# Kernel optimization log

Hardware: AMD Instinct MI355X
Metric: run time of the kernel (lower is better)

The kernel has to match this reference:

```python
import jax, jax.numpy as jnp
from jax import lax
import numpy as np

# kz = (7, 3): kh is a 1x7 horizontal kernel, kv is a 3x1 vertical kernel
KH = (1, 7)
KV = (3, 1)


def _morph(x, ksz, op, init):
    # F.unfold zero-pads, so padded border values participate in the min/max
    ph, pw = ksz[0] // 2, ksz[1] // 2
    xp = jnp.pad(x, ((0, 0), (0, 0), (ph, ph), (pw, pw)))
    return lax.reduce_window(xp, init, op, (1, 1, ksz[0], ksz[1]), (1, 1, 1, 1), 'VALID')


def _erode(x, ksz):
    return _morph(x, ksz, lax.min, np.float32(np.inf))


def _dilate(x, ksz):
    return _morph(x, ksz, lax.max, np.float32(-np.inf))


def _calphi(x):
    dil = _dilate(x, KH)                                   # horizontal dilation (1x7)
    thr = dil.mean(axis=(2, 3), keepdims=True)             # per-image mean of dilation
    bi = ((x > thr) & (x == dil)).astype(x.dtype)          # horizontal local-max binarization
    return _dilate(_erode(bi, KV), KV)                     # morphological opening with 3x1


def setup_inputs() -> dict:
    key = jax.random.key(0)
    x = jax.random.normal(key, (8, 1, 2048, 2048), dtype=jnp.float32)
    return {"x": x}


def reference(x):
    s1 = _calphi(x).sum()
    s2 = _calphi(jnp.swapaxes(x, 2, 3)).sum()
    return s1 < s2
```

## Files before the change

kernel.cpp:

```cpp
#include <hip/hip_runtime.h>
#include <cstdint>

#define NEG_INF (-__builtin_inff())

static constexpr int H = 2048;
static constexpr int W = 2048;
static constexpr int STR = 248;
static constexpr int RC  = 16;
static constexpr int NR  = RC + 6;
static constexpr int NCH = H / RC;
static constexpr int GY  = NCH / 4;
static constexpr int NBLK = 9 * GY * 8;

struct F4 { float x, y, z, w; };

__device__ __forceinline__ F4 ld4(const float* __restrict__ p) {
    float4 v = *reinterpret_cast<const float4*>(p);
    return {v.x, v.y, v.z, v.w};
}

__device__ __forceinline__ float fmax3(float a, float b, float c) {
    return fmaxf(fmaxf(a, b), c);
}

__device__ __forceinline__ void hmax7_4(float a0, float a1, float a2,
                                        float a3, float a4, float a5, float a6,
                                        float a7, float a8, float a9,
                                        float& m0, float& m1, float& m2, float& m3) {
    float p23 = fmaxf(a2, a3), p45 = fmaxf(a4, a5), p67 = fmaxf(a6, a7);
    float q25 = fmaxf(p23, p45), q47 = fmaxf(p45, p67);
    m0 = fmax3(fmaxf(a0, a1), q25, a6);
    m1 = fmax3(fmaxf(a1, a2), fmax3(a3, a4, a5), fmaxf(a6, a7));
    m2 = fmax3(p23, q47, a8);
    m3 = fmax3(fmaxf(a3, a4), fmax3(a5, a6, a7), fmaxf(a8, a9));
}

struct Setup {
    int c4, cA, cmask, imask;
    float pad0, pad1, pad2, pad3;
};

__device__ __forceinline__ Setup make_setup(int sIdx, int lane) {
    Setup s;
    const int cstart = sIdx * STR;
    s.c4 = cstart - 4 + lane * 4;
    s.cA = min(max(s.c4, 0), W - 4);
    s.cmask = 0; s.imask = 0;
#pragma unroll
    for (int k = 0; k < 4; ++k) {
        const int col = s.c4 + k;
        if (col >= cstart && col < cstart + STR && col < W) s.cmask |= 1 << k;
        if (col >= 0 && col < W)                            s.imask |= 1 << k;
    }
    s.pad0 = ((s.c4 + 0) < 3 || (s.c4 + 0) > W - 4) ? 0.f : NEG_INF;
    s.pad1 = ((s.c4 + 1) < 3 || (s.c4 + 1) > W - 4) ? 0.f : NEG_INF;
    s.pad2 = ((s.c4 + 2) < 3 || (s.c4 + 2) > W - 4) ? 0.f : NEG_INF;
    s.pad3 = ((s.c4 + 3) < 3 || (s.c4 + 3) > W - 4) ? 0.f : NEG_INF;
    return s;
}

__device__ __forceinline__ void load_rows(const float* __restrict__ img,
                                          int r0, const Setup& s, F4 (&cur)[NR]) {
#pragma unroll
    for (int t = 0; t < NR; ++t) {
        const int irc = min(max(r0 - 3 + t, 0), H - 1);
        cur[t] = ld4(img + (size_t)irc * W + s.cA);
    }
#pragma unroll
    for (int t = 0; t < NR; ++t)
        asm volatile("" : "+v"(cur[t].x), "+v"(cur[t].y), "+v"(cur[t].z), "+v"(cur[t].w));
    if (s.imask != 0xF) {
#pragma unroll
        for (int t = 0; t < NR; ++t) {
            if (!(s.imask & 1)) cur[t].x = NEG_INF;
            if (!(s.imask & 2)) cur[t].y = NEG_INF;
            if (!(s.imask & 4)) cur[t].z = NEG_INF;
            if (!(s.imask & 8)) cur[t].w = NEG_INF;
        }
    }
#pragma unroll
    for (int t = 0; t < NR; ++t) {
        if (t < 3 || t >= NR - 3) {
            const int ir = r0 - 3 + t;
            if (ir < 0 || ir >= H) cur[t] = {NEG_INF, NEG_INF, NEG_INF, NEG_INF};
        }
    }
}

__device__ __forceinline__ int blk_id() {
    return (blockIdx.z * GY + blockIdx.y) * 9 + blockIdx.x;
}

__global__ __launch_bounds__(256) void k_sums(const float* __restrict__ x,
                                              double* __restrict__ sums) {
    const int tid = threadIdx.x, lane = tid & 63, wid = tid >> 6;
    const int sIdx = blockIdx.x;
    const int rr   = blockIdx.y * 4 + wid;
    const int b    = blockIdx.z;
    const int r0   = rr * RC;
    const float* img = x + (size_t)b * H * W;
    const Setup s = make_setup(sIdx, lane);

    F4 cur[NR];
    load_rows(img, r0, s, cur);

    float shf = 0.f, svf = 0.f;
#pragma unroll
    for (int t = 3; t < 3 + RC; ++t) {
        F4 c = cur[t];
        float la1 = __shfl_up(c.y, 1), la2 = __shfl_up(c.z, 1), la3 = __shfl_up(c.w, 1);
        float ra0 = __shfl_down(c.x, 1), ra1 = __shfl_down(c.y, 1), ra2 = __shfl_down(c.z, 1);
        float m0, m1, m2, m3;
        hmax7_4(la1, la2, la3, c.x, c.y, c.z, c.w, ra0, ra1, ra2, m0, m1, m2, m3);
        m0 = fmaxf(m0, s.pad0); m1 = fmaxf(m1, s.pad1);
        m2 = fmaxf(m2, s.pad2); m3 = fmaxf(m3, s.pad3);
        shf += ((s.cmask & 1) ? m0 : 0.f) + ((s.cmask & 2) ? m1 : 0.f)
             + ((s.cmask & 4) ? m2 : 0.f) + ((s.cmask & 8) ? m3 : 0.f);
    }
#pragma unroll
    for (int jj = 0; jj < RC; ++jj) {
        const int j = r0 + jj;
        const float rpad = (j < 3 || j > H - 4) ? 0.f : NEG_INF;
        float mx = fmax3(fmax3(cur[jj].x, cur[jj+1].x, cur[jj+2].x),
                         fmax3(cur[jj+3].x, cur[jj+4].x, cur[jj+5].x), cur[jj+6].x);
        float my = fmax3(fmax3(cur[jj].y, cur[jj+1].y, cur[jj+2].y),
                         fmax3(cur[jj+3].y, cur[jj+4].y, cur[jj+5].y), cur[jj+6].y);
        float mz = fmax3(fmax3(cur[jj].z, cur[jj+1].z, cur[jj+2].z),
                         fmax3(cur[jj+3].z, cur[jj+4].z, cur[jj+5].z), cur[jj+6].z);
        float mw = fmax3(fmax3(cur[jj].w, cur[jj+1].w, cur[jj+2].w),
                         fmax3(cur[jj+3].w, cur[jj+4].w, cur[jj+5].w), cur[jj+6].w);
        mx = fmaxf(mx, rpad); my = fmaxf(my, rpad);
        mz = fmaxf(mz, rpad); mw = fmaxf(mw, rpad);
        svf += ((s.cmask & 1) ? mx : 0.f) + ((s.cmask & 2) ? my : 0.f)
             + ((s.cmask & 4) ? mz : 0.f) + ((s.cmask & 8) ? mw : 0.f);
    }

    double sh = (double)shf, sv = (double)svf;
    for (int off = 32; off > 0; off >>= 1) {
        sh += __shfl_down(sh, off);
        sv += __shfl_down(sv, off);
    }
    __shared__ double sdh[4], sdv[4];
    if (lane == 0) { sdh[wid] = sh; sdv[wid] = sv; }
    __syncthreads();
    if (tid == 0) {
        const int blk = blk_id();
        sums[blk]        = sdh[0] + sdh[1] + sdh[2] + sdh[3];
        sums[NBLK + blk] = sdv[0] + sdv[1] + sdv[2] + sdv[3];
    }
}

__global__ void k_thr(const double* __restrict__ sums, float* __restrict__ thr) {
    const int tid = threadIdx.x;
    const int pair = tid >> 4, l16 = tid & 15;
    const double* base = sums + (pair < 8 ? pair * 288 : NBLK + (pair - 8) * 288);
    double a = 0.0;
#pragma unroll
    for (int k = 0; k < 18; ++k) a += base[l16 + k * 16];
    a += __shfl_down(a, 8);
    a += __shfl_down(a, 4);
    a += __shfl_down(a, 2);
    a += __shfl_down(a, 1);
    if (l16 == 0) thr[pair] = (float)(a * (1.0 / ((double)H * (double)W)));
}

__global__ __launch_bounds__(256) void k_counts(const float* __restrict__ x,
                                                const float* __restrict__ thr,
                                                unsigned int* __restrict__ cnts) {
    const int tid = threadIdx.x, lane = tid & 63, wid = tid >> 6;
    const int sIdx = blockIdx.x;
    const int rr   = blockIdx.y * 4 + wid;
    const int b    = blockIdx.z;
    const int r0   = rr * RC;
    const float* img = x + (size_t)b * H * W;
    const Setup s = make_setup(sIdx, lane);
    const float thr1 = thr[b], thr2 = thr[8 + b];

    F4 cur[NR];
    load_rows(img, r0, s, cur);

    unsigned bc0 = 0, bc1 = 0, bc2 = 0, bc3 = 0;
#pragma unroll
    for (int t = 1; t < NR - 1; ++t) {
        F4 c = cur[t];
        float la1 = __shfl_up(c.y, 1), la2 = __shfl_up(c.z, 1), la3 = __shfl_up(c.w, 1);
        float ra0 = __shfl_down(c.x, 1), ra1 = __shfl_down(c.y, 1), ra2 = __shfl_down(c.z, 1);
        float m0, m1, m2, m3;
        hmax7_4(la1, la2, la3, c.x, c.y, c.z, c.w, ra0, ra1, ra2, m0, m1, m2, m3);
        m0 = fmaxf(m0, s.pad0); m1 = fmaxf(m1, s.pad1);
        m2 = fmaxf(m2, s.pad2); m3 = fmaxf(m3, s.pad3);
        bc0 |= (c.x > thr1 && c.x == m0) ? (1u << t) : 0u;
        bc1 |= (c.y > thr1 && c.y == m1) ? (1u << t) : 0u;
        bc2 |= (c.z > thr1 && c.z == m2) ? (1u << t) : 0u;
        bc3 |= (c.w > thr1 && c.w == m3) ? (1u << t) : 0u;
    }
    const unsigned rowm = ((1u << RC) - 1u) << 3;
    unsigned e0 = bc0 & (bc0 << 1) & (bc0 >> 1);
    unsigned e1 = bc1 & (bc1 << 1) & (bc1 >> 1);
    unsigned e2 = bc2 & (bc2 << 1) & (bc2 >> 1);
    unsigned e3 = bc3 & (bc3 << 1) & (bc3 >> 1);
    unsigned o0 = e0 | (e0 << 1) | (e0 >> 1);
    unsigned o1_ = e1 | (e1 << 1) | (e1 >> 1);
    unsigned o2_ = e2 | (e2 << 1) | (e2 >> 1);
    unsigned o3_ = e3 | (e3 << 1) | (e3 >> 1);
    unsigned cnt1 = ((s.cmask & 1) ? __popc(o0  & rowm) : 0u)
                  + ((s.cmask & 2) ? __popc(o1_ & rowm) : 0u)
                  + ((s.cmask & 4) ? __popc(o2_ & rowm) : 0u)
                  + ((s.cmask & 8) ? __popc(o3_ & rowm) : 0u);

    unsigned d0 = 0, d1 = 0, d2 = 0, d3 = 0;
#pragma unroll
    for (int jj = 0; jj < RC; ++jj) {
        const int j = r0 + jj;
        const float rpad = (j < 3 || j > H - 4) ? 0.f : NEG_INF;
        float mx = fmax3(fmax3(cur[jj].x, cur[jj+1].x, cur[jj+2].x),
                         fmax3(cur[jj+3].x, cur[jj+4].x, cur[jj+5].x), cur[jj+6].x);
        float my = fmax3(fmax3(cur[jj].y, cur[jj+1].y, cur[jj+2].y),
                         fmax3(cur[jj+3].y, cur[jj+4].y, cur[jj+5].y), cur[jj+6].y);
        float mz = fmax3(fmax3(cur[jj].z, cur[jj+1].z, cur[jj+2].z),
                         fmax3(cur[jj+3].z, cur[jj+4].z, cur[jj+5].z), cur[jj+6].z);
        float mw = fmax3(fmax3(cur[jj].w, cur[jj+1].w, cur[jj+2].w),
                         fmax3(cur[jj+3].w, cur[jj+4].w, cur[jj+5].w), cur[jj+6].w);
        mx = fmaxf(mx, rpad); my = fmaxf(my, rpad);
        mz = fmaxf(mz, rpad); mw = fmaxf(mw, rpad);
        F4 ce = cur[jj + 3];
        d0 |= (ce.x > thr2 && ce.x == mx) ? (1u << jj) : 0u;
        d1 |= (ce.y > thr2 && ce.y == my) ? (1u << jj) : 0u;
        d2 |= (ce.z > thr2 && ce.z == mz) ? (1u << jj) : 0u;
        d3 |= (ce.w > thr2 && ce.w == mw) ? (1u << jj) : 0u;
    }
    const unsigned pz = __shfl_up(d2, 1), pw = __shfl_up(d3, 1);
    const unsigned n0 = __shfl_down(d0, 1), n1 = __shfl_down(d1, 1);
    const unsigned em1 = pz & pw & d0;
    const unsigned f0  = pw & d0 & d1;
    const unsigned f1  = d0 & d1 & d2;
    const unsigned f2  = d1 & d2 & d3;
    const unsigned f3  = d2 & d3 & n0;
    const unsigned fp4 = d3 & n0 & n1;
    const unsigned q0 = em1 | f0 | f1;
    const unsigned q1 = f0 | f1 | f2;
    const unsigned q2 = f1 | f2 | f3;
    const unsigned q3 = f2 | f3 | fp4;
    unsigned cnt2 = ((s.cmask & 1) ? __popc(q0) : 0u)
                  + ((s.cmask & 2) ? __popc(q1) : 0u)
                  + ((s.cmask & 4) ? __popc(q2) : 0u)
                  + ((s.cmask & 8) ? __popc(q3) : 0u);

    for (int off = 32; off > 0; off >>= 1) {
        cnt1 += __shfl_down(cnt1, off);
        cnt2 += __shfl_down(cnt2, off);
    }
    __shared__ unsigned sc1[4], sc2[4];
    if (lane == 0) { sc1[wid] = cnt1; sc2[wid] = cnt2; }
    __syncthreads();
    if (tid == 0) {
        const int blk = blk_id();
        cnts[blk]        = sc1[0] + sc1[1] + sc1[2] + sc1[3];
        cnts[NBLK + blk] = sc2[0] + sc2[1] + sc2[2] + sc2[3];
    }
}

__global__ void k_final(const unsigned int* __restrict__ cnts,
                        int* __restrict__ out) {
    const int tid = threadIdx.x;
    unsigned a = 0, c = 0;
    for (int i = tid; i < NBLK; i += 256) {
        a += cnts[i];
        c += cnts[NBLK + i];
    }
    for (int off = 32; off > 0; off >>= 1) {
        a += __shfl_down(a, off);
        c += __shfl_down(c, off);
    }
    __shared__ unsigned sa[4], sc[4];
    const int lane = tid & 63, wid = tid >> 6;
    if (lane == 0) { sa[wid] = a; sc[wid] = c; }
    __syncthreads();
    if (tid == 0) {
        unsigned A = sa[0] + sa[1] + sa[2] + sa[3];
        unsigned C = sc[0] + sc[1] + sc[2] + sc[3];
        out[0] = (A < C) ? 1 : 0;
    }
}

extern "C" void kernel_launch(void* const* d_in, const int* in_sizes, int n_in,
                              void* d_out, int out_size, void* d_ws, size_t ws_size,
                              hipStream_t stream) {
    const float* x = (const float*)d_in[0];
    int* out = (int*)d_out;
    double* sums = (double*)d_ws;
    float* thr = (float*)((char*)d_ws + 2 * NBLK * 8);
    unsigned int* cnts = (unsigned int*)((char*)d_ws + 2 * NBLK * 8 + 256);

    k_sums  <<<dim3(9, GY, 8), 256, 0, stream>>>(x, sums);
    k_thr   <<<1, 256, 0, stream>>>(sums, thr);
    k_counts<<<dim3(9, GY, 8), 256, 0, stream>>>(x, thr, cnts);
    k_final <<<1, 256, 0, stream>>>(cnts, out);
}
```

Before: 265.3 us.

## Fold threshold and final reductions into main kernels via atomics; halve row chunk

Removes the two single-block kernels (threshold reduction and final count comparison). Per-block partial sums now go through bucketed double and uint atomics, and every k_counts block recomputes the per-image thresholds from 64 buckets. A last-block-done counter in k_counts produces the final comparison, and a memset clears the workspace. The row chunk drops from 16 to 8, doubling the grid and register-friendly work per wave but increasing halo overhead (14 rows loaded per 8 output rows instead of 22 per 16).

New measurement: 621.1 us. 2.34x slower.

```diff
diff --git a/kernel.cpp b/kernel.cpp
--- a/kernel.cpp
+++ b/kernel.cpp
@@ -6,11 +6,10 @@
 static constexpr int H = 2048;
 static constexpr int W = 2048;
 static constexpr int STR = 248;
-static constexpr int RC  = 16;
+static constexpr int RC  = 8;
 static constexpr int NR  = RC + 6;
-static constexpr int NCH = H / RC;
-static constexpr int GY  = NCH / 4;
-static constexpr int NBLK = 9 * GY * 8;
+static constexpr int GY  = (H / RC) / 4;
+static constexpr int NBLOCKS = 9 * GY * 8;
 
 struct F4 { float x, y, z, w; };
 
@@ -85,10 +84,6 @@
             if (ir < 0 || ir >= H) cur[t] = {NEG_INF, NEG_INF, NEG_INF, NEG_INF};
         }
     }
-}
-
-__device__ __forceinline__ int blk_id() {
-    return (blockIdx.z * GY + blockIdx.y) * 9 + blockIdx.x;
 }
 
 __global__ __launch_bounds__(256) void k_sums(const float* __restrict__ x,
@@ -144,37 +139,39 @@
     if (lane == 0) { sdh[wid] = sh; sdv[wid] = sv; }
     __syncthreads();
     if (tid == 0) {
-        const int blk = blk_id();
-        sums[blk]        = sdh[0] + sdh[1] + sdh[2] + sdh[3];
-        sums[NBLK + blk] = sdv[0] + sdv[1] + sdv[2] + sdv[3];
-    }
-}
-
-__global__ void k_thr(const double* __restrict__ sums, float* __restrict__ thr) {
-    const int tid = threadIdx.x;
-    const int pair = tid >> 4, l16 = tid & 15;
-    const double* base = sums + (pair < 8 ? pair * 288 : NBLK + (pair - 8) * 288);
-    double a = 0.0;
-#pragma unroll
-    for (int k = 0; k < 18; ++k) a += base[l16 + k * 16];
-    a += __shfl_down(a, 8);
-    a += __shfl_down(a, 4);
-    a += __shfl_down(a, 2);
-    a += __shfl_down(a, 1);
-    if (l16 == 0) thr[pair] = (float)(a * (1.0 / ((double)H * (double)W)));
+        const int bkt = (blockIdx.y * 9 + sIdx) & 63;
+        atomicAdd(&sums[(b)     * 64 + bkt], sdh[0] + sdh[1] + sdh[2] + sdh[3]);
+        atomicAdd(&sums[(8 + b) * 64 + bkt], sdv[0] + sdv[1] + sdv[2] + sdv[3]);
+    }
 }
 
 __global__ __launch_bounds__(256) void k_counts(const float* __restrict__ x,
-                                                const float* __restrict__ thr,
-                                                unsigned int* __restrict__ cnts) {
+                                                const double* __restrict__ sums,
+                                                unsigned int* __restrict__ cnts,
+                                                unsigned int* __restrict__ done,
+                                                int* __restrict__ out) {
     const int tid = threadIdx.x, lane = tid & 63, wid = tid >> 6;
+    __shared__ float thrS[16];
+
+    {
+        const int pair = tid >> 4, l16 = tid & 15;
+        const double* bp = sums + pair * 64 + l16;
+        double a = bp[0] + bp[16] + bp[32] + bp[48];
+        a += __shfl_down(a, 8);
+        a += __shfl_down(a, 4);
+        a += __shfl_down(a, 2);
+        a += __shfl_down(a, 1);
+        if (l16 == 0) thrS[pair] = (float)(a * (1.0 / ((double)H * (double)W)));
+    }
+    __syncthreads();
+
     const int sIdx = blockIdx.x;
     const int rr   = blockIdx.y * 4 + wid;
     const int b    = blockIdx.z;
     const int r0   = rr * RC;
     const float* img = x + (size_t)b * H * W;
     const Setup s = make_setup(sIdx, lane);
-    const float thr1 = thr[b], thr2 = thr[8 + b];
+    const float thr1 = thrS[b], thr2 = thrS[8 + b];
 
     F4 cur[NR];
     load_rows(img, r0, s, cur);
@@ -199,7 +196,7 @@
     unsigned e1 = bc1 & (bc1 << 1) & (bc1 >> 1);
     unsigned e2 = bc2 & (bc2 << 1) & (bc2 >> 1);
     unsigned e3 = bc3 & (bc3 << 1) & (bc3 >> 1);
-    unsigned o0 = e0 | (e0 << 1) | (e0 >> 1);
+    unsigned o0  = e0 | (e0 << 1) | (e0 >> 1);
     unsigned o1_ = e1 | (e1 << 1) | (e1 >> 1);
     unsigned o2_ = e2 | (e2 << 1) | (e2 >> 1);
     unsigned o3_ = e3 | (e3 << 1) | (e3 >> 1);
@@ -254,32 +251,23 @@
     if (lane == 0) { sc1[wid] = cnt1; sc2[wid] = cnt2; }
     __syncthreads();
     if (tid == 0) {
-        const int blk = blk_id();
-        cnts[blk]        = sc1[0] + sc1[1] + sc1[2] + sc1[3];
-        cnts[NBLK + blk] = sc2[0] + sc2[1] + sc2[2] + sc2[3];
-    }
-}
-
-__global__ void k_final(const unsigned int* __restrict__ cnts,
-                        int* __restrict__ out) {
-    const int tid = threadIdx.x;
-    unsigned a = 0, c = 0;
-    for (int i = tid; i < NBLK; i += 256) {
-        a += cnts[i];
-        c += cnts[NBLK + i];
-    }
-    for (int off = 32; off > 0; off >>= 1) {
-        a += __shfl_down(a, off);
-        c += __shfl_down(c, off);
-    }
-    __shared__ unsigned sa[4], sc[4];
-    const int lane = tid & 63, wid = tid >> 6;
-    if (lane == 0) { sa[wid] = a; sc[wid] = c; }
-    __syncthreads();
-    if (tid == 0) {
-        unsigned A = sa[0] + sa[1] + sa[2] + sa[3];
-        unsigned C = sc[0] + sc[1] + sc[2] + sc[3];
-        out[0] = (A < C) ? 1 : 0;
+        const int bkt = (blockIdx.y * 9 + sIdx) & 63;
+        atomicAdd(&cnts[bkt],      sc1[0] + sc1[1] + sc1[2] + sc1[3]);
+        atomicAdd(&cnts[64 + bkt], sc2[0] + sc2[1] + sc2[2] + sc2[3]);
+    }
+
+    __threadfence();
+    __shared__ unsigned lastFlag;
+    if (tid == 0) lastFlag = (atomicAdd(done, 1u) == NBLOCKS - 1) ? 1u : 0u;
+    __syncthreads();
+    if (lastFlag && tid < 64) {
+        unsigned a = atomicAdd(&cnts[tid], 0u);
+        unsigned c = atomicAdd(&cnts[64 + tid], 0u);
+        for (int off = 32; off > 0; off >>= 1) {
+            a += __shfl_down(a, off);
+            c += __shfl_down(c, off);
+        }
+        if (tid == 0) out[0] = (a < c) ? 1 : 0;
     }
 }
 
@@ -289,11 +277,11 @@
     const float* x = (const float*)d_in[0];
     int* out = (int*)d_out;
     double* sums = (double*)d_ws;
-    float* thr = (float*)((char*)d_ws + 2 * NBLK * 8);
-    unsigned int* cnts = (unsigned int*)((char*)d_ws + 2 * NBLK * 8 + 256);
+    unsigned int* cnts = (unsigned int*)((char*)d_ws + 8192);
+    unsigned int* done = (unsigned int*)((char*)d_ws + 8192 + 512);
+
+    hipMemsetAsync(d_ws, 0, 9216, stream);
 
     k_sums  <<<dim3(9, GY, 8), 256, 0, stream>>>(x, sums);
-    k_thr   <<<1, 256, 0, stream>>>(sums, thr);
-    k_counts<<<dim3(9, GY, 8), 256, 0, stream>>>(x, thr, cnts);
-    k_final <<<1, 256, 0, stream>>>(cnts, out);
-}
+    k_counts<<<dim3(9, GY, 8), 256, 0, stream>>>(x, sums, cnts, done, out);
+}
```
